# Kernel tuning notes

Measured on AMD Instinct MI355X. Metric: run time of the kernel, lower is better.

## Reference

```python
import jax, jax.numpy as jnp
import numpy as np

NUM_BITS = 8
SEQ, BATCH, INPUT, HIDDEN = 512, 256, 256, 256


def fake_quant(w):
    # symmetric per-tensor uniform fake-quantization with straight-through estimator
    qmax = 2.0 ** (NUM_BITS - 1) - 1.0
    scale = jnp.max(jnp.abs(w)) / qmax
    wq = jnp.round(w / scale) * scale
    return w + jax.lax.stop_gradient(wq - w)


def gru_cell(x, h, w_ih, w_hh, b_ih, b_hh):
    # x: [B, I], h: [B, H]; w_ih: [3H, I], w_hh: [3H, H]
    gi = x @ fake_quant(w_ih).T + b_ih  # [B, 3H]
    gh = h @ fake_quant(w_hh).T + b_hh  # [B, 3H]
    i_r, i_z, i_n = jnp.split(gi, 3, axis=-1)
    h_r, h_z, h_n = jnp.split(gh, 3, axis=-1)
    r = jax.nn.sigmoid(i_r + h_r)
    z = jax.nn.sigmoid(i_z + h_z)
    n = jnp.tanh(i_n + r * h_n)
    return (1.0 - z) * n + z * h


def setup_inputs() -> dict:
    key = jax.random.key(0)
    ks = jax.random.split(key, 9)
    s1 = 1.0 / np.sqrt(HIDDEN)
    inp = {
        "x": jax.random.normal(ks[0], (SEQ, BATCH, INPUT), dtype=jnp.float32),
        "h1": jnp.zeros((BATCH, HIDDEN), dtype=jnp.float32),
        "h2": jnp.zeros((BATCH, HIDDEN), dtype=jnp.float32),
        "w_ih1": jax.random.uniform(ks[1], (3 * HIDDEN, INPUT), jnp.float32, -s1, s1),
        "w_hh1": jax.random.uniform(ks[2], (3 * HIDDEN, HIDDEN), jnp.float32, -s1, s1),
        "b_ih1": jax.random.uniform(ks[3], (3 * HIDDEN,), jnp.float32, -s1, s1),
        "b_hh1": jax.random.uniform(ks[4], (3 * HIDDEN,), jnp.float32, -s1, s1),
        "w_ih2": jax.random.uniform(ks[5], (3 * HIDDEN, HIDDEN), jnp.float32, -s1, s1),
        "w_hh2": jax.random.uniform(ks[6], (3 * HIDDEN, HIDDEN), jnp.float32, -s1, s1),
        "b_ih2": jax.random.uniform(ks[7], (3 * HIDDEN,), jnp.float32, -s1, s1),
        "b_hh2": jax.random.uniform(ks[8], (3 * HIDDEN,), jnp.float32, -s1, s1),
    }
    return inp


def reference(x, h1, h2, w_ih1, w_hh1, b_ih1, b_hh1, w_ih2, w_hh2, b_ih2, b_hh2):
    def step(carry, x_t):
        h1, h2 = carry
        h1 = gru_cell(x_t, h1, w_ih1, w_hh1, b_ih1, b_hh1)
        h2 = gru_cell(h1, h2, w_ih2, w_hh2, b_ih2, b_hh2)
        return (h1, h2), None

    (h1, h2), _ = jax.lax.scan(step, (h1, h2), x)
    return h2
```

## Files before the change

### kernel.cpp

```cpp
#include <hip/hip_runtime.h>
#include <hip/hip_fp16.h>
#include <cstdint>

typedef _Float16 half8 __attribute__((ext_vector_type(8)));
typedef _Float16 half4 __attribute__((ext_vector_type(4)));
typedef float f32x4 __attribute__((ext_vector_type(4)));

#define MFMA_F16 __builtin_amdgcn_mfma_f32_16x16x32_f16
#define PIN(x) asm volatile("" : "+v"(x))
#define LD_RLX(p)   __hip_atomic_load((p),  __ATOMIC_RELAXED, __HIP_MEMORY_SCOPE_AGENT)
#define LD_ACQ(p)   __hip_atomic_load((p),  __ATOMIC_ACQUIRE, __HIP_MEMORY_SCOPE_AGENT)
#define ST_REL(p,v) __hip_atomic_store((p),(v), __ATOMIC_RELEASE, __HIP_MEMORY_SCOPE_AGENT)

__device__ __forceinline__ float fast_rcp(float x){
#if __has_builtin(__builtin_amdgcn_rcpf)
  return __builtin_amdgcn_rcpf(x);
#else
  return 1.0f/x;
#endif
}
__device__ __forceinline__ float fast_exp2(float x){
#if __has_builtin(__builtin_amdgcn_exp2f)
  return __builtin_amdgcn_exp2f(x);
#else
  return exp2f(x);
#endif
}
__device__ __forceinline__ float sigm_f(float x){
  return fast_rcp(1.0f + fast_exp2(-1.44269504f*x));
}
__device__ __forceinline__ float tanh_fast(float x){
  float e = fast_exp2(-2.88539008f*x);
  return fmaf(2.0f, fast_rcp(1.0f + e), -1.0f);
}

__device__ __forceinline__ void bar_weak(){
  asm volatile("s_waitcnt lgkmcnt(0)" ::: "memory");
  __builtin_amdgcn_s_barrier();
  asm volatile("" ::: "memory");
}
__device__ __forceinline__ void bar_strong(){
  asm volatile("s_waitcnt vmcnt(0) lgkmcnt(0)" ::: "memory");
  __builtin_amdgcn_s_barrier();
  asm volatile("" ::: "memory");
}

__global__ __launch_bounds__(256) void k_maxabs(
    const float* __restrict__ w0, const float* __restrict__ w1,
    const float* __restrict__ w2, const float* __restrict__ w3,
    int n, int* __restrict__ slots)
{
  const float* srcs[4] = {w0, w1, w2, w3};
  int m    = blockIdx.x >> 5;
  int part = blockIdx.x & 31;
  const float* w = srcs[m];
  float loc = 0.0f;
  for (int i = part*256 + threadIdx.x; i < n; i += 32*256)
    loc = fmaxf(loc, fabsf(w[i]));
  for (int off = 32; off; off >>= 1)
    loc = fmaxf(loc, __shfl_down(loc, off, 64));
  __shared__ float red[4];
  int wv = threadIdx.x >> 6;
  if ((threadIdx.x & 63) == 0) red[wv] = loc;
  __syncthreads();
  if (threadIdx.x == 0) {
    float mx = fmaxf(fmaxf(red[0], red[1]), fmaxf(red[2], red[3]));
    atomicMax(&slots[m], __float_as_int(mx));
  }
}

__global__ __launch_bounds__(256) void k_quant(
    const float* __restrict__ w0, const float* __restrict__ w1,
    const float* __restrict__ w2, const float* __restrict__ w3,
    const int* __restrict__ slots,
    _Float16* __restrict__ f0, _Float16* __restrict__ f1,
    _Float16* __restrict__ f2, _Float16* __restrict__ f3)
{
  const float* srcs[4] = {w0, w1, w2, w3};
  _Float16*    dsts[4] = {f0, f1, f2, f3};
  int idx = blockIdx.x*256 + threadIdx.x;
  int m = idx / 196608;
  int e = idx - m*196608;
  float scale = __int_as_float(slots[m]) * (1.0f/127.0f);
  float w = srcs[m][e];
  float q = rintf(w/scale) * scale;
  int g = e >> 8, k = e & 255;
  int tile = g >> 4, kb = k >> 5;
  int lane = ((k >> 3) & 3)*16 + (g & 15);
  int off  = (tile*8 + kb)*512 + lane*8 + (k & 7);
  dsts[m][off] = (_Float16)q;
}

__global__ __launch_bounds__(256) void k_gemm_f32(
    const float* __restrict__ A, const _Float16* __restrict__ Wf,
    const float* __restrict__ bih, const float* __restrict__ bhh,
    _Float16* __restrict__ gi)
{
  __shared__ _Float16 Al[16384];
  const int tid = threadIdx.x;
  const long r0 = (long)blockIdx.x * 64;
  const int by  = blockIdx.y;

  const float4* A4 = (const float4*)A;
  #pragma unroll
  for (int p = 0; p < 16; p++) {
    int n = p*256 + tid;
    int row = n >> 6, f4 = n & 63, k0 = f4*4;
    float4 v = A4[(r0 + row)*64 + f4];
    int lane = ((k0 >> 3) & 3)*16 + (row & 15);
    _Float16* d = &Al[((row >> 4)*8 + (k0 >> 5))*512 + lane*8 + (k0 & 7)];
    d[0] = (_Float16)v.x; d[1] = (_Float16)v.y;
    d[2] = (_Float16)v.z; d[3] = (_Float16)v.w;
  }
  __syncthreads();

  const int w = tid >> 6, l = tid & 63, c16 = l & 15;
  f32x4 acc[8];
  #pragma unroll
  for (int nt = 0; nt < 8; nt++) acc[nt] = (f32x4){0.f, 0.f, 0.f, 0.f};
  float bv[8];
  #pragma unroll
  for (int nt = 0; nt < 8; nt++) {
    int col = by*128 + nt*16 + c16;
    bv[nt] = bih[col] + (col < 512 ? bhh[col] : 0.0f);
  }

  #pragma unroll
  for (int kb = 0; kb < 8; kb++) {
    half8 a = *(const half8*)&Al[(w*8 + kb)*512 + l*8];
    #pragma unroll
    for (int nt = 0; nt < 8; nt++) {
      half8 b = *(const half8*)&Wf[((size_t)((by*8 + nt)*8 + kb))*512 + l*8];
      acc[nt] = MFMA_F16(a, b, acc[nt], 0, 0, 0);
    }
  }

  const int t = (int)(r0 >> 8);
  const int bb = ((int)(r0 & 255) >> 4) + w;
  #pragma unroll
  for (int nt = 0; nt < 8; nt++) {
    int cj = by*8 + nt;
    int g  = cj >> 4, jw = cj & 15;
    size_t chunk = ((size_t)t*16 + jw)*16 + bb;
    half4 v;
    #pragma unroll
    for (int i = 0; i < 4; i++) v[i] = (_Float16)(acc[nt][i] + bv[nt]);
    *(half4*)&gi[chunk*768 + l*12 + g*4] = v;
  }
}

__global__ __launch_bounds__(512, 2) void k_pipe(
    const _Float16* __restrict__ gi1, const _Float16* __restrict__ wfhh1,
    const float* __restrict__ bhh1, float* __restrict__ hc1,
    _Float16* __restrict__ h1seq,
    const _Float16* __restrict__ wfih2, const float* __restrict__ bih2,
    const float* __restrict__ bhh2, const _Float16* __restrict__ wfhh2,
    float* __restrict__ hc2, _Float16* __restrict__ gi2,
    int* __restrict__ flag1, int* __restrict__ flag2, int* __restrict__ flag3)
{
  __shared__ __align__(16) _Float16 hl[2][4096];
  __shared__ __align__(16) _Float16 wn_l[16384];
  const int role = blockIdx.x;
  const int tid  = threadIdx.x;
  const int w = tid >> 6, l = tid & 63, q = l >> 4, c16 = l & 15;

  if (role >= 32) {
    const int id = role - 32, bb = id >> 1, par = id & 1;
    float bR[2], bZ[2], bN[2];
    half8 wr[2][8], wz[2][8], wn[2][8];
    #pragma unroll
    for (int nt = 0; nt < 2; nt++) {
      const int j = w*32 + nt*16 + c16;
      bR[nt] = bih2[j]       + bhh2[j];
      bZ[nt] = bih2[256 + j] + bhh2[256 + j];
      bN[nt] = bih2[512 + j];
      const _Float16* WR = wfih2 + (size_t)(2*w + nt)      *4096;
      const _Float16* WZ = wfih2 + (size_t)(16 + 2*w + nt) *4096;
      const _Float16* WN = wfih2 + (size_t)(32 + 2*w + nt) *4096;
      #pragma unroll
      for (int kb = 0; kb < 8; kb++) {
        wr[nt][kb] = *(const half8*)&WR[(kb*64 + l)*8];  PIN(wr[nt][kb]);
        wz[nt][kb] = *(const half8*)&WZ[(kb*64 + l)*8];  PIN(wz[nt][kb]);
        wn[nt][kb] = *(const half8*)&WN[(kb*64 + l)*8];  PIN(wn[nt][kb]);
      }
    }

    for (int g = par; g < 32; g += 2) {
      const int t0 = g*16;
      if (tid == 0) {
        while (LD_RLX(&flag1[bb]) < t0 + 16) __builtin_amdgcn_s_sleep(10);
        if (g >= 4)
          while (LD_RLX(&flag3[bb]) < (g - 3)*16) __builtin_amdgcn_s_sleep(10);
        (void)LD_ACQ(&flag1[bb]);
      }
      __syncthreads();
      for (int t = t0; t < t0 + 16; t++) {
        const _Float16* ap = h1seq + (size_t)t*65536 + (size_t)bb*4096 + l*8;
        f32x4 aR[2], aZ[2], aN[2];
        #pragma unroll
        for (int nt = 0; nt < 2; nt++) {
          aR[nt] = (f32x4){0.f,0.f,0.f,0.f};
          aZ[nt] = (f32x4){0.f,0.f,0.f,0.f};
          aN[nt] = (f32x4){0.f,0.f,0.f,0.f};
        }
        #pragma unroll
        for (int kb = 0; kb < 8; kb++) {
          half8 a = *(const half8*)&ap[kb*512];
          #pragma unroll
          for (int nt = 0; nt < 2; nt++) {
            aR[nt] = MFMA_F16(a, wr[nt][kb], aR[nt], 0, 0, 0);
            aZ[nt] = MFMA_F16(a, wz[nt][kb], aZ[nt], 0, 0, 0);
            aN[nt] = MFMA_F16(a, wn[nt][kb], aN[nt], 0, 0, 0);
          }
        }
        #pragma unroll
        for (int nt = 0; nt < 2; nt++) {
          _Float16* op = gi2 + ((size_t)(t & 63)*256 + (2*w + nt)*16 + bb)*768 + l*12;
          half4 vR, vZ, vN;
          #pragma unroll
          for (int i = 0; i < 4; i++) {
            vR[i] = (_Float16)(aR[nt][i] + bR[nt]);
            vZ[i] = (_Float16)(aZ[nt][i] + bZ[nt]);
            vN[i] = (_Float16)(aN[nt][i] + bN[nt]);
          }
          *(half4*)(op)     = vR;
          *(half4*)(op + 4) = vZ;
          *(half4*)(op + 8) = vN;
        }
      }
      __syncthreads();
      if (tid == 0) ST_REL(&flag2[bb*2 + par], t0 + 16);
    }
    return;
  }

  const bool L1 = (role < 16);
  const int bb = L1 ? role : role - 16;
  const int b0 = bb * 16;
  const _Float16* gi = L1 ? gi1 : gi2;
  const _Float16* Wf = L1 ? wfhh1 : wfhh2;
  const float* bhh   = L1 ? bhh1 : bhh2;
  float* hcarry      = L1 ? hc1 : hc2;

  {
    int n = tid*8;
    int b = n >> 8, k = n & 255;
    const float4* s4 = (const float4*)&hcarry[(size_t)(b0 + b)*256 + k];
    float4 v0 = s4[0], v1 = s4[1];
    half8 hv;
    hv[0] = (_Float16)v0.x; hv[1] = (_Float16)v0.y;
    hv[2] = (_Float16)v0.z; hv[3] = (_Float16)v0.w;
    hv[4] = (_Float16)v1.x; hv[5] = (_Float16)v1.y;
    hv[6] = (_Float16)v1.z; hv[7] = (_Float16)v1.w;
    *(half8*)&hl[0][(k >> 5)*512 + (((k >> 3) & 3)*16 + b)*8] = hv;
  }

  float bN[2];
  float hprev[2][4];
  half8 wr[2][8], wz[2][8], wn[2][6];
  int   wr_off[2];
  int   gil[2];
  #pragma unroll
  for (int nt = 0; nt < 2; nt++) {
    const int j = w*32 + nt*16 + c16;
    bN[nt] = bhh[512 + j];
    #pragma unroll
    for (int i = 0; i < 4; i++)
      hprev[nt][i] = hcarry[(size_t)(b0 + q*4 + i)*256 + j];
    const _Float16* WR = Wf + (size_t)(2*w + nt)      *4096;
    const _Float16* WZ = Wf + (size_t)(16 + 2*w + nt) *4096;
    const _Float16* WN = Wf + (size_t)(32 + 2*w + nt) *4096;
    #pragma unroll
    for (int kb = 0; kb < 8; kb++) {
      wr[nt][kb] = *(const half8*)&WR[(kb*64 + l)*8];  PIN(wr[nt][kb]);
      wz[nt][kb] = *(const half8*)&WZ[(kb*64 + l)*8];  PIN(wz[nt][kb]);
    }
    #pragma unroll
    for (int kb = 2; kb < 8; kb++) {
      wn[nt][kb-2] = *(const half8*)&WN[(kb*64 + l)*8];  PIN(wn[nt][kb-2]);
    }
    #pragma unroll
    for (int kb = 0; kb < 2; kb++)
      *(half8*)&wn_l[((w*2 + nt)*2 + kb)*512 + l*8] =
          *(const half8*)&WN[(kb*64 + l)*8];
    wr_off[nt] = (j >> 5)*512 + ((j >> 3) & 3)*128 + (j & 7);
    gil[nt]    = ((2*w + nt)*16 + bb)*768 + l*12;
  }
  _Float16* hq = L1 ? (h1seq + (size_t)bb*4096 + tid*8) : (_Float16*)nullptr;

  __syncthreads();
  int cur = 0;
  for (int t = 0; t < 512; t++) {
    if (!L1 && (t & 15) == 0) {
      if (tid == 0) {
        int* f = &flag2[bb*2 + ((t >> 4) & 1)];
        while (LD_RLX(f) < t + 16) __builtin_amdgcn_s_sleep(10);
        (void)LD_ACQ(f);
      }
      __syncthreads();
    }
    const int tm = L1 ? t : (t & 63);
    const _Float16* gbase = gi + (size_t)tm*196608;
    half4 vR[2], vZ[2], vN[2];
    #pragma unroll
    for (int nt = 0; nt < 2; nt++) {
      const _Float16* gp = gbase + gil[nt];
      vR[nt] = *(const half4*)(gp);
      vZ[nt] = *(const half4*)(gp + 4);
      vN[nt] = *(const half4*)(gp + 8);
    }

    f32x4 aR[2], aZ[2], aN[2];
    #pragma unroll
    for (int nt = 0; nt < 2; nt++) {
      aR[nt] = (f32x4){0.f,0.f,0.f,0.f};
      aZ[nt] = (f32x4){0.f,0.f,0.f,0.f};
      aN[nt] = (f32x4){0.f,0.f,0.f,0.f};
    }
    #pragma unroll
    for (int kb = 0; kb < 8; kb++) {
      half8 a = *(const half8*)&hl[cur][kb*512 + l*8];
      #pragma unroll
      for (int nt = 0; nt < 2; nt++) {
        half8 bn = (kb < 2)
            ? *(const half8*)&wn_l[((w*2 + nt)*2 + kb)*512 + l*8]
            : wn[nt][kb-2];
        aR[nt] = MFMA_F16(a, wr[nt][kb], aR[nt], 0, 0, 0);
        aZ[nt] = MFMA_F16(a, wz[nt][kb], aZ[nt], 0, 0, 0);
        aN[nt] = MFMA_F16(a, bn,         aN[nt], 0, 0, 0);
      }
    }

    const int nxt = cur ^ 1;
    #pragma unroll
    for (int nt = 0; nt < 2; nt++) {
      #pragma unroll
      for (int i = 0; i < 4; i++) {
        float r  = sigm_f(aR[nt][i] + (float)vR[nt][i]);
        float z  = sigm_f(aZ[nt][i] + (float)vZ[nt][i]);
        float nn = tanh_fast((float)vN[nt][i] + r*(aN[nt][i] + bN[nt]));
        float hp = nn + z*(hprev[nt][i] - nn);
        hprev[nt][i] = hp;
        hl[nxt][wr_off[nt] + (q*4 + i)*8] = (_Float16)hp;
      }
    }

    if ((t & 15) == 0 && t > 0) {
      bar_strong();
      if (tid == 0) {
        if (L1) ST_REL(&flag1[bb], t);
        else    ST_REL(&flag3[bb], t);
      }
    } else {
      bar_weak();
    }
    if (L1)
      *(half8*)&hq[(size_t)t*65536] = *(const half8*)&hl[nxt][tid*8];
    cur = nxt;
  }
  bar_strong();
  if (tid == 0) {
    if (L1) ST_REL(&flag1[bb], 512);
    else    ST_REL(&flag3[bb], 512);
  }

  #pragma unroll
  for (int nt = 0; nt < 2; nt++) {
    const int j = w*32 + nt*16 + c16;
    #pragma unroll
    for (int i = 0; i < 4; i++)
      hcarry[(size_t)(b0 + q*4 + i)*256 + j] = hprev[nt][i];
  }
}

extern "C" void kernel_launch(void* const* d_in, const int* in_sizes, int n_in,
                              void* d_out, int out_size, void* d_ws, size_t ws_size,
                              hipStream_t stream)
{
  const float* x     = (const float*)d_in[0];
  const float* h1_0  = (const float*)d_in[1];
  const float* h2_0  = (const float*)d_in[2];
  const float* w_ih1 = (const float*)d_in[3];
  const float* w_hh1 = (const float*)d_in[4];
  const float* b_ih1 = (const float*)d_in[5];
  const float* b_hh1 = (const float*)d_in[6];
  const float* w_ih2 = (const float*)d_in[7];
  const float* w_hh2 = (const float*)d_in[8];
  const float* b_ih2 = (const float*)d_in[9];
  const float* b_hh2 = (const float*)d_in[10];

  char* ws = (char*)d_ws;
  size_t off = 0;
  auto alloc = [&](size_t bytes) -> void* {
    void* p = ws + off; off += (bytes + 255) & ~(size_t)255; return p;
  };
  int*      slots   = (int*)     alloc(16);
  _Float16* wf_ih1  = (_Float16*)alloc(196608*2);
  _Float16* wf_hh1  = (_Float16*)alloc(196608*2);
  _Float16* wf_ih2  = (_Float16*)alloc(196608*2);
  _Float16* wf_hh2  = (_Float16*)alloc(196608*2);
  float*    hc1     = (float*)   alloc(256*256*4);
  float*    hc2     = (float*)   alloc(256*256*4);
  int*      flag1   = (int*)     alloc(16*4);
  int*      flag2   = (int*)     alloc(32*4);
  int*      flag3   = (int*)     alloc(16*4);
  _Float16* gi1     = (_Float16*)alloc((size_t)512*393216);
  _Float16* h1seq   = (_Float16*)alloc((size_t)512*131072);
  _Float16* gi2     = (_Float16*)alloc((size_t)64*393216);

  k_maxabs<<<128, 256, 0, stream>>>(w_ih1, w_hh1, w_ih2, w_hh2, 196608, slots);
  k_quant <<<3072, 256, 0, stream>>>(w_ih1, w_hh1, w_ih2, w_hh2, slots,
                                     wf_ih1, wf_hh1, wf_ih2, wf_hh2);
  (void)hipMemcpyAsync(hc1, h1_0, 256*256*4, hipMemcpyDeviceToDevice, stream);
  (void)hipMemcpyAsync(hc2, h2_0, 256*256*4, hipMemcpyDeviceToDevice, stream);

  dim3 gg(2048, 6);
  k_gemm_f32<<<gg, 256, 0, stream>>>(x, wf_ih1, b_ih1, b_hh1, gi1);

  k_pipe<<<64, 512, 0, stream>>>(gi1, wf_hh1, b_hh1, hc1, h1seq,
                                 wf_ih2, b_ih2, b_hh2, wf_hh2,
                                 hc2, gi2, flag1, flag2, flag3);

  (void)hipMemcpyAsync(d_out, hc2, 256*256*4, hipMemcpyDeviceToDevice, stream);
}
```

Before: 1.598 ms.

## Fuse layer-1 input projection into persistent pipeline kernel with flag handoff

Removes the separate layer-1 input GEMM kernel and adds 32 producer blocks to the persistent pipeline kernel. These blocks compute gi1 for 16-timestep chunks from x and publish progress through new flag0 counters, so the layer-1 recurrence consumes chunks as they are produced instead of waiting for the whole GEMM. It also prefetches the next timestep's gate inputs into registers during the MFMA loop. The cost is more resident blocks, extra spin-wait synchronisation, and added register pressure from the prefetch. flag0 is never reset in the shown host code, which may break correctness across repeated calls.

```diff
diff --git a/kernel.cpp b/kernel.cpp
--- a/kernel.cpp
+++ b/kernel.cpp
@@ -91,78 +91,94 @@
   dsts[m][off] = (_Float16)q;
 }
 
-__global__ __launch_bounds__(256) void k_gemm_f32(
-    const float* __restrict__ A, const _Float16* __restrict__ Wf,
-    const float* __restrict__ bih, const float* __restrict__ bhh,
-    _Float16* __restrict__ gi)
-{
-  __shared__ _Float16 Al[16384];
-  const int tid = threadIdx.x;
-  const long r0 = (long)blockIdx.x * 64;
-  const int by  = blockIdx.y;
-
-  const float4* A4 = (const float4*)A;
-  #pragma unroll
-  for (int p = 0; p < 16; p++) {
-    int n = p*256 + tid;
-    int row = n >> 6, f4 = n & 63, k0 = f4*4;
-    float4 v = A4[(r0 + row)*64 + f4];
-    int lane = ((k0 >> 3) & 3)*16 + (row & 15);
-    _Float16* d = &Al[((row >> 4)*8 + (k0 >> 5))*512 + lane*8 + (k0 & 7)];
-    d[0] = (_Float16)v.x; d[1] = (_Float16)v.y;
-    d[2] = (_Float16)v.z; d[3] = (_Float16)v.w;
-  }
-  __syncthreads();
-
-  const int w = tid >> 6, l = tid & 63, c16 = l & 15;
-  f32x4 acc[8];
-  #pragma unroll
-  for (int nt = 0; nt < 8; nt++) acc[nt] = (f32x4){0.f, 0.f, 0.f, 0.f};
-  float bv[8];
-  #pragma unroll
-  for (int nt = 0; nt < 8; nt++) {
-    int col = by*128 + nt*16 + c16;
-    bv[nt] = bih[col] + (col < 512 ? bhh[col] : 0.0f);
-  }
-
-  #pragma unroll
-  for (int kb = 0; kb < 8; kb++) {
-    half8 a = *(const half8*)&Al[(w*8 + kb)*512 + l*8];
-    #pragma unroll
-    for (int nt = 0; nt < 8; nt++) {
-      half8 b = *(const half8*)&Wf[((size_t)((by*8 + nt)*8 + kb))*512 + l*8];
-      acc[nt] = MFMA_F16(a, b, acc[nt], 0, 0, 0);
-    }
-  }
-
-  const int t = (int)(r0 >> 8);
-  const int bb = ((int)(r0 & 255) >> 4) + w;
-  #pragma unroll
-  for (int nt = 0; nt < 8; nt++) {
-    int cj = by*8 + nt;
-    int g  = cj >> 4, jw = cj & 15;
-    size_t chunk = ((size_t)t*16 + jw)*16 + bb;
-    half4 v;
-    #pragma unroll
-    for (int i = 0; i < 4; i++) v[i] = (_Float16)(acc[nt][i] + bv[nt]);
-    *(half4*)&gi[chunk*768 + l*12 + g*4] = v;
-  }
-}
-
 __global__ __launch_bounds__(512, 2) void k_pipe(
-    const _Float16* __restrict__ gi1, const _Float16* __restrict__ wfhh1,
+    const float* __restrict__ x,
+    const _Float16* __restrict__ wfih1, const float* __restrict__ bih1,
+    _Float16* __restrict__ gi1, const _Float16* __restrict__ wfhh1,
     const float* __restrict__ bhh1, float* __restrict__ hc1,
     _Float16* __restrict__ h1seq,
     const _Float16* __restrict__ wfih2, const float* __restrict__ bih2,
     const float* __restrict__ bhh2, const _Float16* __restrict__ wfhh2,
     float* __restrict__ hc2, _Float16* __restrict__ gi2,
-    int* __restrict__ flag1, int* __restrict__ flag2, int* __restrict__ flag3)
+    int* __restrict__ flag0, int* __restrict__ flag1,
+    int* __restrict__ flag2, int* __restrict__ flag3)
 {
   __shared__ __align__(16) _Float16 hl[2][4096];
   __shared__ __align__(16) _Float16 wn_l[16384];
   const int role = blockIdx.x;
   const int tid  = threadIdx.x;
   const int w = tid >> 6, l = tid & 63, q = l >> 4, c16 = l & 15;
+
+  if (role >= 64) {
+    const int id = role - 64, bb = id >> 1, par = id & 1;
+    const int b0 = bb * 16;
+    float bR[2], bZ[2], bN[2];
+    half8 wr[2][8], wz[2][8], wn[2][8];
+    #pragma unroll
+    for (int nt = 0; nt < 2; nt++) {
+      const int j = w*32 + nt*16 + c16;
+      bR[nt] = bih1[j]       + bhh1[j];
+      bZ[nt] = bih1[256 + j] + bhh1[256 + j];
+      bN[nt] = bih1[512 + j];
+      const _Float16* WR = wfih1 + (size_t)(2*w + nt)      *4096;
+      const _Float16* WZ = wfih1 + (size_t)(16 + 2*w + nt) *4096;
+      const _Float16* WN = wfih1 + (size_t)(32 + 2*w + nt) *4096;
+      #pragma unroll
+      for (int kb = 0; kb < 8; kb++) {
+        wr[nt][kb] = *(const half8*)&WR[(kb*64 + l)*8];  PIN(wr[nt][kb]);
+        wz[nt][kb] = *(const half8*)&WZ[(kb*64 + l)*8];  PIN(wz[nt][kb]);
+        wn[nt][kb] = *(const half8*)&WN[(kb*64 + l)*8];  PIN(wn[nt][kb]);
+      }
+    }
+    const float* xb = x + (size_t)(b0 + (l & 15))*256 + (l >> 4)*8;
+
+    for (int g = par; g < 32; g += 2) {
+      const int t0 = g*16;
+      for (int t = t0; t < t0 + 16; t++) {
+        const float* xp = xb + (size_t)t*65536;
+        f32x4 aR[2], aZ[2], aN[2];
+        #pragma unroll
+        for (int nt = 0; nt < 2; nt++) {
+          aR[nt] = (f32x4){0.f,0.f,0.f,0.f};
+          aZ[nt] = (f32x4){0.f,0.f,0.f,0.f};
+          aN[nt] = (f32x4){0.f,0.f,0.f,0.f};
+        }
+        #pragma unroll
+        for (int kb = 0; kb < 8; kb++) {
+          float4 f0 = *(const float4*)(xp + kb*32);
+          float4 f1 = *(const float4*)(xp + kb*32 + 4);
+          half8 a;
+          a[0] = (_Float16)f0.x; a[1] = (_Float16)f0.y;
+          a[2] = (_Float16)f0.z; a[3] = (_Float16)f0.w;
+          a[4] = (_Float16)f1.x; a[5] = (_Float16)f1.y;
+          a[6] = (_Float16)f1.z; a[7] = (_Float16)f1.w;
+          #pragma unroll
+          for (int nt = 0; nt < 2; nt++) {
+            aR[nt] = MFMA_F16(a, wr[nt][kb], aR[nt], 0, 0, 0);
+            aZ[nt] = MFMA_F16(a, wz[nt][kb], aZ[nt], 0, 0, 0);
+            aN[nt] = MFMA_F16(a, wn[nt][kb], aN[nt], 0, 0, 0);
+          }
+        }
+        #pragma unroll
+        for (int nt = 0; nt < 2; nt++) {
+          _Float16* op = gi1 + ((size_t)t*256 + (2*w + nt)*16 + bb)*768 + l*12;
+          half4 vR, vZ, vN;
+          #pragma unroll
+          for (int i = 0; i < 4; i++) {
+            vR[i] = (_Float16)(aR[nt][i] + bR[nt]);
+            vZ[i] = (_Float16)(aZ[nt][i] + bZ[nt]);
+            vN[i] = (_Float16)(aN[nt][i] + bN[nt]);
+          }
+          *(half4*)(op)     = vR;
+          *(half4*)(op + 4) = vZ;
+          *(half4*)(op + 8) = vN;
+        }
+      }
+      __syncthreads();
+      if (tid == 0) ST_REL(&flag0[bb*2 + par], t0 + 16);
+    }
+    return;
+  }
 
   if (role >= 32) {
     const int id = role - 32, bb = id >> 1, par = id & 1;
@@ -289,25 +305,31 @@
   _Float16* hq = L1 ? (h1seq + (size_t)bb*4096 + tid*8) : (_Float16*)nullptr;
 
   __syncthreads();
+  half4 pR[2], pZ[2], pN[2];
   int cur = 0;
   for (int t = 0; t < 512; t++) {
-    if (!L1 && (t & 15) == 0) {
+    if ((t & 15) == 0) {
       if (tid == 0) {
-        int* f = &flag2[bb*2 + ((t >> 4) & 1)];
+        int* f = L1 ? &flag0[bb*2 + ((t >> 4) & 1)]
+                    : &flag2[bb*2 + ((t >> 4) & 1)];
         while (LD_RLX(f) < t + 16) __builtin_amdgcn_s_sleep(10);
         (void)LD_ACQ(f);
       }
       __syncthreads();
-    }
-    const int tm = L1 ? t : (t & 63);
-    const _Float16* gbase = gi + (size_t)tm*196608;
+      const int tm = L1 ? t : (t & 63);
+      const _Float16* gbase = gi + (size_t)tm*196608;
+      #pragma unroll
+      for (int nt = 0; nt < 2; nt++) {
+        const _Float16* gp = gbase + gil[nt];
+        pR[nt] = *(const half4*)(gp);
+        pZ[nt] = *(const half4*)(gp + 4);
+        pN[nt] = *(const half4*)(gp + 8);
+      }
+    }
     half4 vR[2], vZ[2], vN[2];
     #pragma unroll
     for (int nt = 0; nt < 2; nt++) {
-      const _Float16* gp = gbase + gil[nt];
-      vR[nt] = *(const half4*)(gp);
-      vZ[nt] = *(const half4*)(gp + 4);
-      vN[nt] = *(const half4*)(gp + 8);
+      vR[nt] = pR[nt]; vZ[nt] = pZ[nt]; vN[nt] = pN[nt];
     }
 
     f32x4 aR[2], aZ[2], aN[2];
@@ -328,6 +350,18 @@
         aR[nt] = MFMA_F16(a, wr[nt][kb], aR[nt], 0, 0, 0);
         aZ[nt] = MFMA_F16(a, wz[nt][kb], aZ[nt], 0, 0, 0);
         aN[nt] = MFMA_F16(a, bn,         aN[nt], 0, 0, 0);
+      }
+    }
+
+    if (((t + 1) & 15) != 0) {
+      const int tn = L1 ? (t + 1) : ((t + 1) & 63);
+      const _Float16* gbase = gi + (size_t)tn*196608;
+      #pragma unroll
+      for (int nt = 0; nt < 2; nt++) {
+        const _Float16* gp = gbase + gil[nt];
+        pR[nt] = *(const half4*)(gp);
+        pZ[nt] = *(const half4*)(gp + 4);
+        pN[nt] = *(const half4*)(gp + 8);
       }
     }
 
@@ -401,6 +435,7 @@
   _Float16* wf_hh2  = (_Float16*)alloc(196608*2);
   float*    hc1     = (float*)   alloc(256*256*4);
   float*    hc2     = (float*)   alloc(256*256*4);
+  int*      flag0   = (int*)     alloc(32*4);
   int*      flag1   = (int*)     alloc(16*4);
   int*      flag2   = (int*)     alloc(32*4);
   int*      flag3   = (int*)     alloc(16*4);
@@ -414,12 +449,9 @@
   (void)hipMemcpyAsync(hc1, h1_0, 256*256*4, hipMemcpyDeviceToDevice, stream);
   (void)hipMemcpyAsync(hc2, h2_0, 256*256*4, hipMemcpyDeviceToDevice, stream);
 
-  dim3 gg(2048, 6);
-  k_gemm_f32<<<gg, 256, 0, stream>>>(x, wf_ih1, b_ih1, b_hh1, gi1);
-
-  k_pipe<<<64, 512, 0, stream>>>(gi1, wf_hh1, b_hh1, hc1, h1seq,
-                                 wf_ih2, b_ih2, b_hh2, wf_hh2,
-                                 hc2, gi2, flag1, flag2, flag3);
+  k_pipe<<<96, 512, 0, stream>>>(x, wf_ih1, b_ih1, gi1, wf_hh1, b_hh1,
+                                 hc1, h1seq, wf_ih2, b_ih2, b_hh2, wf_hh2,
+                                 hc2, gi2, flag0, flag1, flag2, flag3);
 
   (void)hipMemcpyAsync(d_out, hc2, 256*256*4, hipMemcpyDeviceToDevice, stream);
 }
```

Measured after the change: 1.571 ms. Within noise of the previous version (-1.7%).
